# Optimization experiments

Hardware: AMD Instinct MI355X
Metric: run time of the kernel (lower is better)

Reference implementation:

```python
import jax, jax.numpy as jnp
import numpy as np

N_VERTS = 200000
N_TETS = 800000
FREQ_NUM = 4
SCALE = 1.0
HID = 256
D_IN = 3 + 6 * FREQ_NUM  # 27

_TRI_TABLE = np.array([
    [-1,-1,-1,-1,-1,-1],[1,0,2,-1,-1,-1],[4,0,3,-1,-1,-1],[1,4,2,1,3,4],
    [3,1,5,-1,-1,-1],[2,3,0,2,5,3],[1,4,0,1,5,4],[4,2,5,-1,-1,-1],
    [4,5,2,-1,-1,-1],[4,1,0,4,5,1],[3,2,0,3,5,2],[1,3,5,-1,-1,-1],
    [4,1,2,4,3,1],[3,0,4,-1,-1,-1],[2,0,1,-1,-1,-1],[-1,-1,-1,-1,-1,-1]], dtype=np.int32)
_NUM_TRI = np.array([0,1,1,2,1,2,2,1,1,2,2,1,2,1,1,0], dtype=np.int32)
_BASE_EDGES = np.array([0,1,0,2,0,3,1,2,1,3,2,3], dtype=np.int32)


def _pos_enc(x):
    feats = [x]
    for i in range(FREQ_NUM):
        f = float(2 ** i) * np.pi / SCALE
        feats.append(jnp.sin(f * x))
        feats.append(jnp.cos(f * x))
    return jnp.concatenate(feats, axis=-1)  # [N, 27]


def _mlp_sdf(pos, w0, b0, w1, b1, w2, b2, w3, b3, wf, bf):
    h = jax.nn.relu(_pos_enc(pos) @ w0 + b0)
    for w, b in ((w1, b1), (w2, b2), (w3, b3)):
        h = jax.nn.relu(h @ w + b)
    return (h @ wf + bf)[:, 0]  # [N]


def setup_inputs() -> dict:
    key = jax.random.key(0)
    ks = jax.random.split(key, 12)
    def lin(k, fan_in, shape):
        return jax.random.normal(k, shape, jnp.float32) * (2.0 / fan_in) ** 0.5
    return {
        "pos": jax.random.normal(ks[0], (N_VERTS, 3), jnp.float32),
        "tet_fx4": jax.random.randint(ks[1], (N_TETS, 4), 0, N_VERTS, dtype=jnp.int32),
        "w0": lin(ks[2], D_IN, (D_IN, HID)), "b0": jnp.zeros((HID,), jnp.float32),
        "w1": lin(ks[3], HID, (HID, HID)), "b1": jnp.zeros((HID,), jnp.float32),
        "w2": lin(ks[4], HID, (HID, HID)), "b2": jnp.zeros((HID,), jnp.float32),
        "w3": lin(ks[5], HID, (HID, HID)), "b3": jnp.zeros((HID,), jnp.float32),
        "wf": lin(ks[6], HID, (HID, 1)), "bf": jnp.zeros((1,), jnp.float32),
    }


def reference(pos, tet_fx4, w0, b0, w1, b1, w2, b2, w3, b3, wf, bf):
    # SDF from the positional-encoding MLP (DMTetGeometry)
    sdf = _mlp_sdf(pos, w0, b0, w1, b1, w2, b2, w3, b3, wf, bf)

    # --- marching tetrahedra (DMTet.__call__) ---
    occ = sdf > 0                       # [N]
    occ_fx4 = occ[tet_fx4]              # [F,4]
    occ_sum = occ_fx4.sum(-1)
    valid = (occ_sum > 0) & (occ_sum < 4)
    vt = tet_fx4[valid]                 # [V,4] tets crossed by the surface
    occ_v = occ_fx4[valid]              # [V,4]

    # all 6 edges per valid tet, sorted so (lo, hi)
    e = vt[:, _BASE_EDGES].reshape(-1, 2)                         # [6V,2]
    e = jnp.stack([jnp.minimum(e[:, 0], e[:, 1]),
                   jnp.maximum(e[:, 0], e[:, 1])], axis=1)
    uniq, inv = jnp.unique(e, axis=0, return_inverse=True)        # dedup edges
    inv = inv.reshape(-1)

    # edges whose endpoints straddle the zero level set
    cross = occ[uniq].sum(-1) == 1                                 # [U]
    mapping = jnp.where(cross, jnp.cumsum(cross) - 1, -1)          # compact ids
    idx_map = mapping[inv].reshape(-1, 6)                          # [V,6]
    interp_v = uniq[cross]                                         # [M,2]

    # linear interpolation of crossing vertices along each crossing edge
    p = pos[interp_v]                                              # [M,2,3]
    s = sdf[interp_v]                                              # [M,2]
    denom = s[:, 0] - s[:, 1]                                      # s0 + (-s1)
    verts = (p[:, 0] * (-s[:, 1])[:, None] + p[:, 1] * s[:, 0][:, None]) / denom[:, None]

    # triangle table lookup
    tetindex = (occ_v.astype(jnp.int32) * (2 ** jnp.arange(4, dtype=jnp.int32))).sum(-1)
    ntri = jnp.asarray(_NUM_TRI)[tetindex]
    tri = jnp.asarray(_TRI_TABLE)[tetindex]
    m1 = ntri == 1
    m2 = ntri == 2
    f1 = jnp.take_along_axis(idx_map[m1], tri[m1][:, :3], axis=1).reshape(-1, 3)
    f2 = jnp.take_along_axis(idx_map[m2], tri[m2][:, :6], axis=1).reshape(-1, 3)
    faces = jnp.concatenate([f1, f2], axis=0)
    return verts, faces
```

## Files before the change

### kernel.cpp

```cpp
#include <hip/hip_runtime.h>
#include <cstdint>
#include <cstddef>

#define NV 200000
#define NT 800000
#define ROWS 64
#define MBLK 3125
#define NBLK 3125
#define NSEGS 196
#define PCAP 4096
#define AST 264
#define PST (ROWS*AST)

typedef unsigned int u32;
typedef unsigned long long u64;

typedef __attribute__((ext_vector_type(8))) _Float16 half8;
typedef __attribute__((ext_vector_type(4))) float f32x4;
typedef __attribute__((ext_vector_type(16))) float f32x16;
#define MFMA32F __builtin_amdgcn_mfma_f32_32x32x16_f16

__constant__ int c_tri[16][6] = {
  {-1,-1,-1,-1,-1,-1},{1,0,2,-1,-1,-1},{4,0,3,-1,-1,-1},{1,4,2,1,3,4},
  {3,1,5,-1,-1,-1},{2,3,0,2,5,3},{1,4,0,1,5,4},{4,2,5,-1,-1,-1},
  {4,5,2,-1,-1,-1},{4,1,0,4,5,1},{3,2,0,3,5,2},{1,3,5,-1,-1,-1},
  {4,1,2,4,3,1},{3,0,4,-1,-1,-1},{2,0,1,-1,-1,-1},{-1,-1,-1,-1,-1,-1}};
__constant__ int c_ntri[16] = {0,1,1,2,1,2,2,1,1,2,2,1,2,1,1,0};
__constant__ int c_be[12] = {0,1,0,2,0,3,1,2,1,3,2,3};

__device__ __forceinline__ void split2(float x, _Float16& h, _Float16& m){
  h = (_Float16)x;
  const float r = x - (float)h;
  m = (_Float16)(r * 2048.0f);
}

__global__ void split_weights(const float* __restrict__ w0, const float* __restrict__ w1,
                              const float* __restrict__ w2, const float* __restrict__ w3,
                              _Float16* __restrict__ wp, u32* __restrict__ segcur)
{
  const int t = blockIdx.x*256 + threadIdx.x;
  if (t < 256) segcur[t] = 0u;
  int base, psz, c, kg, n, kvalid;
  const float* w;
  if (t < 1024){
    base = 0; psz = 8192;
    c = t >> 9; kg = (t >> 8) & 1; n = t & 255;
    w = w0; kvalid = 27;
  } else {
    int r = t - 1024;
    const int l = r >> 13;
    r &= 8191;
    c = r >> 9; kg = (r >> 8) & 1; n = r & 255;
    base = 16384 + l*131072; psz = 65536;
    w = (l==0) ? w1 : (l==1) ? w2 : w3;
    kvalid = 256;
  }
  half8 hv, mv;
#pragma unroll
  for (int j=0;j<8;j++){
    const int k = c*16 + kg*8 + j;
    const float val = (k < kvalid) ? w[k*256 + n] : 0.f;
    _Float16 h, m; split2(val, h, m);
    hv[j] = h; mv[j] = m;
  }
  const int off = (c*256 + n)*16 + kg*8;
  *(half8*)(wp + base + off) = hv;
  *(half8*)(wp + base + psz + off) = mv;
}

template<int NCH, int PSZ, bool LAST>
__device__ __forceinline__ void layer_run(
    const _Float16* __restrict__ Wl, const float* __restrict__ Bv,
    const float* __restrict__ wfv,
    _Float16 (*Af)[ROWS][AST], float (*part)[5],
    int lane, int wv)
{
  const int l31 = lane & 31, hi = lane >> 5;
  const int rt = wv >> 2, cg = wv & 3;
  const int col0 = cg * 64;
  f32x16 g0[2], g1[2];
#pragma unroll
  for (int nt=0; nt<2; nt++){
#pragma unroll
    for (int r=0; r<16; r++){ g0[nt][r] = 0.f; g1[nt][r] = 0.f; }
  }

  const _Float16* bp = Wl + (u32)((col0 + l31)*16 + hi*8);
  half8 bA[2][2], bB[2][2];

  auto loadB = [&](int c, half8 (*dst)[2]){
#pragma unroll
    for (int p=0;p<2;p++)
#pragma unroll
      for (int nt=0;nt<2;nt++)
        dst[p][nt] = *(const half8*)(bp + p*PSZ + c*4096 + nt*512);
  };
  auto compute = [&](int c, const half8 (*bb)[2]){
    const _Float16* ap = &Af[0][rt*32 + l31][c*16 + hi*8];
    const half8 ah = *(const half8*)(ap);
    const half8 am = *(const half8*)(ap + PST);
#pragma unroll
    for (int nt=0;nt<2;nt++){
      g0[nt] = MFMA32F(ah, bb[0][nt], g0[nt], 0,0,0);
      g1[nt] = MFMA32F(ah, bb[1][nt], g1[nt], 0,0,0);
      g1[nt] = MFMA32F(am, bb[0][nt], g1[nt], 0,0,0);
    }
  };

  loadB(0, bA);
#pragma unroll 1
  for (int ch=0; ch<NCH/2; ch++){
    const int c0 = 2*ch;
    loadB(c0+1, bB);
    compute(c0, bA);
    if (c0+2 < NCH) loadB(c0+2, bA);
    compute(c0+1, bB);
  }
  __syncthreads();

  const float S = 4.8828125e-4f;
  if (!LAST){
#pragma unroll
    for (int nt=0;nt<2;nt++){
      const int col = col0 + nt*32 + l31;
      const float bias = Bv[col];
#pragma unroll
      for (int reg=0;reg<16;reg++){
        const int row = rt*32 + (reg&3) + 8*(reg>>2) + 4*hi;
        const float v = fmaxf(g0[nt][reg] + S*g1[nt][reg] + bias, 0.f);
        _Float16 h,m; split2(v,h,m);
        Af[0][row][col] = h; Af[1][row][col] = m;
      }
    }
  } else {
    float pr[16];
#pragma unroll
    for (int reg=0;reg<16;reg++) pr[reg] = 0.f;
#pragma unroll
    for (int nt=0;nt<2;nt++){
      const int col = col0 + nt*32 + l31;
      const float bias = Bv[col];
      const float w = wfv[col];
#pragma unroll
      for (int reg=0;reg<16;reg++)
        pr[reg] += fmaxf(g0[nt][reg] + S*g1[nt][reg] + bias, 0.f) * w;
    }
#pragma unroll
    for (int s=1;s<32;s<<=1)
#pragma unroll
      for (int reg=0;reg<16;reg++)
        pr[reg] += __shfl_xor(pr[reg], s, 64);
    if (l31 == 0){
#pragma unroll
      for (int reg=0;reg<16;reg++)
        part[rt*32 + (reg&3) + 8*(reg>>2) + 4*hi][cg] = pr[reg];
    }
  }
  __syncthreads();
}

__global__ __launch_bounds__(512,4) void mlp_mfma(
    const float* __restrict__ pos, const _Float16* __restrict__ wp,
    const float* __restrict__ b0, const float* __restrict__ b1,
    const float* __restrict__ b2, const float* __restrict__ b3,
    const float* __restrict__ wf, const float* __restrict__ bf,
    float* __restrict__ sdf)
{
  __shared__ _Float16 Af[2][ROWS][AST];
  __shared__ float part[ROWS][5];
  const int tid = threadIdx.x;
  const int lane = tid & 63, wv = tid >> 6;
  const int row0 = blockIdx.x * ROWS;

#pragma unroll
  for (int it=0; it<4; it++){
    const int idx = it*512 + tid;
    const int r = idx & 63, f = idx >> 6;
    float val = 0.f;
    if (f < 3){
      val = pos[(row0 + r)*3 + f];
    } else if (f < 27){
      const int g = (f-3)/6, rem = (f-3)%6;
      const int d = rem % 3;
      const float x = pos[(row0 + r)*3 + d];
      const float fr = (float)(1 << g) * 3.14159265358979323846f;
      val = (rem < 3) ? sinf(fr*x) : cosf(fr*x);
    }
    _Float16 h,m; split2(val,h,m);
    Af[0][r][f] = h; Af[1][r][f] = m;
  }
  __syncthreads();

  layer_run< 2,  8192,false>(wp + 0,      b0, nullptr, Af, part, lane, wv);
  layer_run<16, 65536,false>(wp + 16384,  b1, nullptr, Af, part, lane, wv);
  layer_run<16, 65536,false>(wp + 147456, b2, nullptr, Af, part, lane, wv);
  layer_run<16, 65536,true >(wp + 278528, b3, wf,      Af, part, lane, wv);

  if (tid < ROWS){
    float s = part[tid][0] + part[tid][1] + part[tid][2] + part[tid][3];
    sdf[row0 + tid] = s + bf[0];
  }
}

__device__ __forceinline__ u32 wave_scan_incl(u32 v, int lane){
#pragma unroll
  for (int s=1;s<64;s<<=1){
    const u32 y = __shfl_up(v, s, 64);
    if (lane >= s) v += y;
  }
  return v;
}
__device__ __forceinline__ u32 block_scan_fast(u32 v, u32* sh4, int tid){
  const int lane = tid & 63, wv = tid >> 6;
  const u32 incl = wave_scan_incl(v, lane);
  if (lane == 63) sh4[wv] = incl;
  __syncthreads();
  u32 base = 0;
#pragma unroll
  for (int w=0;w<3;w++) if (w < wv) base += sh4[w];
  return incl + base;
}
__device__ __forceinline__ u64 bscan_u64(u64 v, u64* sh, int tid){
  sh[tid]=v; __syncthreads();
#pragma unroll
  for (int s=1;s<256;s<<=1){
    const u64 y = (tid>=s) ? sh[tid-s] : 0ull;
    __syncthreads();
    sh[tid] += y;
    __syncthreads();
  }
  return sh[tid];
}

__global__ void tet_pairs(const int* __restrict__ tet, const float* __restrict__ sdf,
    unsigned char* __restrict__ codes, u32* __restrict__ tscan, u32* __restrict__ tsum,
    u32* __restrict__ segcur, u64* __restrict__ pairs)
{
  __shared__ u32 sh4[4];
  const int tid = threadIdx.x;
  const int t = blockIdx.x*256 + tid;
  const int4 v = *(const int4*)(&tet[4*t]);
  const int o0 = sdf[v.x] > 0.f;
  const int o1 = sdf[v.y] > 0.f;
  const int o2 = sdf[v.z] > 0.f;
  const int o3 = sdf[v.w] > 0.f;
  const int code = o0 | (o1<<1) | (o2<<2) | (o3<<3);
  codes[t] = (unsigned char)code;
  const int nt = c_ntri[code];
  if (nt > 0){
    const int vv[4] = {v.x, v.y, v.z, v.w};
    const int oc[4] = {o0,o1,o2,o3};
#pragma unroll
    for (int e=0;e<6;e++){
      const int ia = c_be[2*e], ib = c_be[2*e+1];
      if (oc[ia] != oc[ib]){
        const int p = vv[ia], q = vv[ib];
        const int lo = p<q ? p : q, hi = p<q ? q : p;
        const int seg = lo >> 10;
        const u32 slot = atomicAdd(&segcur[seg], 1u);
        if (slot < PCAP)
          pairs[(size_t)seg*PCAP + slot] = ((u64)(u32)lo << 32) | (u32)hi;
      }
    }
  }
  const u32 my = (u32)(nt==1) | ((u32)(nt==2)<<16);
  const u32 incl = block_scan_fast(my, sh4, tid);
  tscan[t] = incl - my;
  if (tid == 255) tsum[blockIdx.x] = incl;
}

__global__ void seg_process(const u64* __restrict__ pairs_in, const u32* __restrict__ segcur,
    u64* __restrict__ uq, u32* __restrict__ ucnt, u32* __restrict__ ucnt_ex,
    u32* __restrict__ usum, const u32* __restrict__ tsum, u64* __restrict__ tsumE,
    u32* __restrict__ meta)
{
  const int tid = threadIdx.x;
  if (blockIdx.x == NSEGS){
    __shared__ u64 sh64[256];
    u64 loc[13]; u64 tot = 0ull;
#pragma unroll
    for (int i=0;i<13;i++){
      const int idx = tid*13 + i;
      const u32 p = (idx < NBLK) ? tsum[idx] : 0u;
      const u64 u = (u64)(p & 0xffffu) | ((u64)(p >> 16) << 32);
      loc[i] = u; tot += u;
    }
    const u64 incl = bscan_u64(tot, sh64, tid);
    u64 run = incl - tot;
#pragma unroll
    for (int i=0;i<13;i++){
      const int idx = tid*13 + i;
      if (idx < NBLK) tsumE[idx] = run;
      run += loc[i];
    }
    if (tid == 255){ meta[0] = (u32)(incl & 0xffffffffull); meta[1] = (u32)(incl >> 32); }
    return;
  }

  __shared__ u64 P[PCAP];
  __shared__ u32 sh4[4];
  __shared__ u32 shbase;
  const int seg = blockIdx.x;
  int n = (int)segcur[seg];
  if (n > PCAP) n = PCAP;
  int np = 1; while (np < n) np <<= 1;

  for (int i=tid; i<np; i+=256)
    P[i] = (i < n) ? pairs_in[(size_t)seg*PCAP + i] : ~0ull;
  if (tid == 0) shbase = 0u;
  __syncthreads();

  for (int k=2; k<=np; k<<=1){
    for (int j=k>>1; j>0; j>>=1){
      for (int i=tid; i<np; i+=256){
        const int ij = i ^ j;
        if (ij > i){
          const u64 a = P[i], b = P[ij];
          const bool up = ((i & k) == 0);
          if ((a > b) == up){ P[i] = b; P[ij] = a; }
        }
      }
      __syncthreads();
    }
  }

  for (int c=0; c<n; c+=256){
    const int i = c + tid;
    u64 key = 0ull; u32 f = 0u;
    if (i < n){
      key = P[i];
      f = (i == 0 || P[i] != P[i-1]) ? 1u : 0u;
    }
    __syncthreads();
    const u32 incl = block_scan_fast(f, sh4, tid);
    const u32 base = shbase;
    if (f) P[base + incl - 1u] = key;
    __syncthreads();
    if (tid == 255) shbase = base + incl;
    __syncthreads();
  }
  const int uc = (int)shbase;

  for (int i=tid; i<uc; i+=256) uq[(size_t)seg*PCAP + i] = P[i];

  const int lo0 = seg << 10;
  for (int c=0; c<1024; c+=256){
    const int lo = lo0 + c + tid;
    if (lo < NV){
      const u64 kl = (u64)(u32)lo << 32;
      const u64 kh = (u64)(u32)(lo+1) << 32;
      int a=0, b=uc;
      while (a < b){ const int m=(a+b)>>1; if (P[m] < kl) a=m+1; else b=m; }
      const int lb = a;
      b = uc;
      while (a < b){ const int m=(a+b)>>1; if (P[m] < kh) a=m+1; else b=m; }
      ucnt_ex[lo] = (u32)lb;
      ucnt[lo] = (u32)(a - lb);
    }
  }
  if (tid == 0) usum[seg] = (u32)uc;
}

__global__ void emit_all(const int* __restrict__ tet, const float* __restrict__ pos,
    const float* __restrict__ sdf, const unsigned char* __restrict__ codes,
    const u32* __restrict__ tscan, const u64* __restrict__ tsumE, const u32* __restrict__ meta,
    const u64* __restrict__ uq, const u32* __restrict__ ucnt, const u32* __restrict__ ucnt_ex,
    const u32* __restrict__ usum, float* __restrict__ out, int out_size)
{
  __shared__ u32 sh4[4];
  __shared__ u32 shu[NSEGS];
  __shared__ u32 shM;
  const int tid = threadIdx.x;
  {
    const u32 v = (tid < NSEGS) ? usum[tid] : 0u;
    const u32 incl = block_scan_fast(v, sh4, tid);
    if (tid < NSEGS) shu[tid] = incl - v;
    if (tid == NSEGS-1) shM = incl;
    __syncthreads();
  }

  if (blockIdx.x < NSEGS){
    const int seg = blockIdx.x;
    const int uc = (int)usum[seg];
    const u32 base = shu[seg];
    for (int i=tid; i<uc; i+=256){
      const u64 key = uq[(size_t)seg*PCAP + i];
      const int lo = (int)(key >> 32);
      const int hi = (int)(key & 0xffffffffull);
      const float s0 = sdf[lo], s1 = sdf[hi];
      const float d = s0 - s1;
      const float vx = (pos[3*lo  ]*(-s1) + pos[3*hi  ]*s0) / d;
      const float vy = (pos[3*lo+1]*(-s1) + pos[3*hi+1]*s0) / d;
      const float vz = (pos[3*lo+2]*(-s1) + pos[3*hi+2]*s0) / d;
      const long long w = 3ll*(long long)(base + (u32)i);
      if (w + 3 <= (long long)out_size){
        out[w] = vx; out[w+1] = vy; out[w+2] = vz;
      }
    }
  } else {
    const int t = (blockIdx.x - NSEGS)*256 + tid;
    const int code = codes[t];
    const int nt = c_ntri[code];
    if (nt == 0) return;
    const u64 tb = tsumE[t>>8];
    const u32 ts = tscan[t];
    const u32 n1e = (u32)(tb & 0xffffffffull) + (ts & 0xffffu);
    const u32 n2e = (u32)(tb >> 32) + (ts >> 16);
    const u32 N1 = meta[0];
    const u32 M  = shM;
    const u32 fb = (nt==1) ? n1e : (N1 + 2u*n2e);
    const int4 v = *(const int4*)(&tet[4*t]);
    const int vv[4] = {v.x, v.y, v.z, v.w};
    for (int r=0;r<nt;r++){
      for (int k=0;k<3;k++){
        const int e = c_tri[code][3*r+k];
        const int ia = c_be[2*e], ib = c_be[2*e+1];
        const int p = vv[ia], q = vv[ib];
        const int lo = p<q ? p : q, hi = p<q ? q : p;
        const int seg = lo >> 10;
        const u32 st = ucnt_ex[lo];
        const int u = (int)ucnt[lo];
        const u64* b = uq + (size_t)seg*PCAP + st;
        int id = -1;
        for (int j=0;j<u;j++){
          if ((int)(b[j] & 0xffffffffull) == hi){ id = (int)(shu[seg] + st) + j; break; }
        }
        const long long w = 3ll*(long long)M + 3ll*(long long)(fb + (u32)r) + k;
        if (w < (long long)out_size && id >= 0) out[w] = (float)id;
      }
    }
  }
}

extern "C" void kernel_launch(void* const* d_in, const int* in_sizes, int n_in,
                              void* d_out, int out_size, void* d_ws, size_t ws_size,
                              hipStream_t stream)
{
  (void)in_sizes; (void)n_in; (void)ws_size;
  const float* pos = (const float*)d_in[0];
  const int*   tet = (const int*)d_in[1];
  const float* w0 = (const float*)d_in[2];
  const float* b0 = (const float*)d_in[3];
  const float* w1 = (const float*)d_in[4];
  const float* b1 = (const float*)d_in[5];
  const float* w2 = (const float*)d_in[6];
  const float* b2 = (const float*)d_in[7];
  const float* w3 = (const float*)d_in[8];
  const float* b3 = (const float*)d_in[9];
  const float* wf = (const float*)d_in[10];
  const float* bf = (const float*)d_in[11];
  float* out = (float*)d_out;
  char* ws = (char*)d_ws;

  float*         sdf   = (float*)(ws + 0);
  unsigned char* codes = (unsigned char*)(ws + 800000);
  u32* tscan   = (u32*)(ws + 1600000);
  u32* tsum    = (u32*)(ws + 4800000);
  u64* tsumE   = (u64*)(ws + 4812800);
  u32* segcur  = (u32*)(ws + 4837888);
  u32* usum    = (u32*)(ws + 4838912);
  u32* meta    = (u32*)(ws + 4839936);
  u32* ucnt    = (u32*)(ws + 4840000);
  u32* ucnt_ex = (u32*)(ws + 5640000);
  _Float16* wp = (_Float16*)(ws + 6440000);
  u64* pairs   = (u64*)(ws + 7259200);

  split_weights<<<100,256,0,stream>>>(w0,w1,w2,w3,wp,segcur);
  mlp_mfma<<<MBLK,512,0,stream>>>(pos,wp,b0,b1,b2,b3,wf,bf,sdf);

  tet_pairs<<<NBLK,256,0,stream>>>(tet,sdf,codes,tscan,tsum,segcur,pairs);
  seg_process<<<NSEGS+1,256,0,stream>>>(pairs,segcur,pairs,ucnt,ucnt_ex,usum,tsum,tsumE,meta);
  emit_all<<<NSEGS+NBLK,256,0,stream>>>(tet,pos,sdf,codes,tscan,tsumE,meta,
                                        pairs,ucnt,ucnt_ex,usum,out,out_size);
}
```

Baseline: 497.5 us.

## Remap MLP waves to column strips and add 32-row tail blocks

Each of the 8 waves now owns a 32-column strip and loops over all row tiles, so every B weight fragment loaded from global memory is reused across two row tiles instead of each wave loading two column tiles. This halves per-wave weight loads while increasing A-fragment LDS reads. The grid is split into 3072 full 64-row blocks plus 106 half-size 32-row blocks, so the last wave of blocks is finer-grained and work spreads more evenly across CUs. Partial sums are now reduced across 8 waves instead of 4.

```diff
diff --git a/kernel.cpp b/kernel.cpp
--- a/kernel.cpp
+++ b/kernel.cpp
@@ -5,18 +5,17 @@
 #define NV 200000
 #define NT 800000
 #define ROWS 64
-#define MBLK 3125
+#define MAINB 3072
+#define TAILB 106
+#define MBLK (MAINB+TAILB)
 #define NBLK 3125
 #define NSEGS 196
 #define PCAP 4096
-#define AST 264
-#define PST (ROWS*AST)
 
 typedef unsigned int u32;
 typedef unsigned long long u64;
 
 typedef __attribute__((ext_vector_type(8))) _Float16 half8;
-typedef __attribute__((ext_vector_type(4))) float f32x4;
 typedef __attribute__((ext_vector_type(16))) float f32x16;
 #define MFMA32F __builtin_amdgcn_mfma_f32_32x32x16_f16
 
@@ -68,42 +67,38 @@
   *(half8*)(wp + base + psz + off) = mv;
 }
 
-template<int NCH, int PSZ, bool LAST>
+template<int RT, int NCH, int PSZ, bool LAST>
 __device__ __forceinline__ void layer_run(
     const _Float16* __restrict__ Wl, const float* __restrict__ Bv,
     const float* __restrict__ wfv,
-    _Float16 (*Af)[ROWS][AST], float (*part)[5],
+    _Float16* __restrict__ Af, float (*part)[8],
     int lane, int wv)
 {
   const int l31 = lane & 31, hi = lane >> 5;
-  const int rt = wv >> 2, cg = wv & 3;
-  const int col0 = cg * 64;
-  f32x16 g0[2], g1[2];
-#pragma unroll
-  for (int nt=0; nt<2; nt++){
-#pragma unroll
-    for (int r=0; r<16; r++){ g0[nt][r] = 0.f; g1[nt][r] = 0.f; }
-  }
+  const int col0 = wv * 32;
+  constexpr u32 PSTl = (u32)(RT*32*264);
+  f32x16 g0[RT], g1[RT];
+#pragma unroll
+  for (int i=0;i<RT;i++)
+#pragma unroll
+    for (int r=0;r<16;r++){ g0[i][r] = 0.f; g1[i][r] = 0.f; }
 
   const _Float16* bp = Wl + (u32)((col0 + l31)*16 + hi*8);
-  half8 bA[2][2], bB[2][2];
-
-  auto loadB = [&](int c, half8 (*dst)[2]){
-#pragma unroll
-    for (int p=0;p<2;p++)
-#pragma unroll
-      for (int nt=0;nt<2;nt++)
-        dst[p][nt] = *(const half8*)(bp + p*PSZ + c*4096 + nt*512);
+  half8 bA[2], bB[2];
+
+  auto loadB = [&](int c, half8* dst){
+    dst[0] = *(const half8*)(bp + c*4096);
+    dst[1] = *(const half8*)(bp + PSZ + c*4096);
   };
-  auto compute = [&](int c, const half8 (*bb)[2]){
-    const _Float16* ap = &Af[0][rt*32 + l31][c*16 + hi*8];
-    const half8 ah = *(const half8*)(ap);
-    const half8 am = *(const half8*)(ap + PST);
-#pragma unroll
-    for (int nt=0;nt<2;nt++){
-      g0[nt] = MFMA32F(ah, bb[0][nt], g0[nt], 0,0,0);
-      g1[nt] = MFMA32F(ah, bb[1][nt], g1[nt], 0,0,0);
-      g1[nt] = MFMA32F(am, bb[0][nt], g1[nt], 0,0,0);
+  auto compute = [&](int c, const half8* bb){
+#pragma unroll
+    for (int rt=0;rt<RT;rt++){
+      const _Float16* ap = Af + (u32)((rt*32 + l31)*264 + c*16 + hi*8);
+      const half8 ah = *(const half8*)(ap);
+      const half8 am = *(const half8*)(ap + PSTl);
+      g0[rt] = MFMA32F(ah, bb[0], g0[rt], 0,0,0);
+      g1[rt] = MFMA32F(ah, bb[1], g1[rt], 0,0,0);
+      g1[rt] = MFMA32F(am, bb[0], g1[rt], 0,0,0);
     }
   };
 
@@ -119,44 +114,56 @@
   __syncthreads();
 
   const float S = 4.8828125e-4f;
+  const int col = col0 + l31;
   if (!LAST){
-#pragma unroll
-    for (int nt=0;nt<2;nt++){
-      const int col = col0 + nt*32 + l31;
-      const float bias = Bv[col];
+    const float bias = Bv[col];
+#pragma unroll
+    for (int rt=0;rt<RT;rt++)
 #pragma unroll
       for (int reg=0;reg<16;reg++){
         const int row = rt*32 + (reg&3) + 8*(reg>>2) + 4*hi;
-        const float v = fmaxf(g0[nt][reg] + S*g1[nt][reg] + bias, 0.f);
+        const float v = fmaxf(g0[rt][reg] + S*g1[rt][reg] + bias, 0.f);
         _Float16 h,m; split2(v,h,m);
-        Af[0][row][col] = h; Af[1][row][col] = m;
+        Af[(u32)(row*264 + col)] = h;
+        Af[PSTl + (u32)(row*264 + col)] = m;
       }
-    }
   } else {
-    float pr[16];
-#pragma unroll
-    for (int reg=0;reg<16;reg++) pr[reg] = 0.f;
-#pragma unroll
-    for (int nt=0;nt<2;nt++){
-      const int col = col0 + nt*32 + l31;
-      const float bias = Bv[col];
-      const float w = wfv[col];
+    const float bias = Bv[col];
+    const float w = wfv[col];
+    float pr[RT][16];
+#pragma unroll
+    for (int rt=0;rt<RT;rt++)
 #pragma unroll
       for (int reg=0;reg<16;reg++)
-        pr[reg] += fmaxf(g0[nt][reg] + S*g1[nt][reg] + bias, 0.f) * w;
-    }
+        pr[rt][reg] = fmaxf(g0[rt][reg] + S*g1[rt][reg] + bias, 0.f) * w;
 #pragma unroll
     for (int s=1;s<32;s<<=1)
 #pragma unroll
-      for (int reg=0;reg<16;reg++)
-        pr[reg] += __shfl_xor(pr[reg], s, 64);
+      for (int rt=0;rt<RT;rt++)
+#pragma unroll
+        for (int reg=0;reg<16;reg++)
+          pr[rt][reg] += __shfl_xor(pr[rt][reg], s, 64);
     if (l31 == 0){
 #pragma unroll
-      for (int reg=0;reg<16;reg++)
-        part[rt*32 + (reg&3) + 8*(reg>>2) + 4*hi][cg] = pr[reg];
+      for (int rt=0;rt<RT;rt++)
+#pragma unroll
+        for (int reg=0;reg<16;reg++)
+          part[rt*32 + (reg&3) + 8*(reg>>2) + 4*hi][wv] = pr[rt][reg];
     }
   }
   __syncthreads();
+}
+
+__device__ __forceinline__ float posenc_val(const float* __restrict__ pos, int gr, int f){
+  if (f < 3) return pos[gr*3 + f];
+  if (f < 27){
+    const int g = (f-3)/6, rem = (f-3)%6;
+    const int d = rem % 3;
+    const float x = pos[gr*3 + d];
+    const float fr = (float)(1 << g) * 3.14159265358979323846f;
+    return (rem < 3) ? sinf(fr*x) : cosf(fr*x);
+  }
+  return 0.f;
 }
 
 __global__ __launch_bounds__(512,4) void mlp_mfma(
@@ -166,39 +173,60 @@
     const float* __restrict__ wf, const float* __restrict__ bf,
     float* __restrict__ sdf)
 {
-  __shared__ _Float16 Af[2][ROWS][AST];
-  __shared__ float part[ROWS][5];
+  __shared__ _Float16 Af[2*ROWS*264];
+  __shared__ float part[ROWS][8];
   const int tid = threadIdx.x;
   const int lane = tid & 63, wv = tid >> 6;
-  const int row0 = blockIdx.x * ROWS;
-
-#pragma unroll
-  for (int it=0; it<4; it++){
-    const int idx = it*512 + tid;
-    const int r = idx & 63, f = idx >> 6;
-    float val = 0.f;
-    if (f < 3){
-      val = pos[(row0 + r)*3 + f];
-    } else if (f < 27){
-      const int g = (f-3)/6, rem = (f-3)%6;
-      const int d = rem % 3;
-      const float x = pos[(row0 + r)*3 + d];
-      const float fr = (float)(1 << g) * 3.14159265358979323846f;
-      val = (rem < 3) ? sinf(fr*x) : cosf(fr*x);
-    }
-    _Float16 h,m; split2(val,h,m);
-    Af[0][r][f] = h; Af[1][r][f] = m;
-  }
-  __syncthreads();
-
-  layer_run< 2,  8192,false>(wp + 0,      b0, nullptr, Af, part, lane, wv);
-  layer_run<16, 65536,false>(wp + 16384,  b1, nullptr, Af, part, lane, wv);
-  layer_run<16, 65536,false>(wp + 147456, b2, nullptr, Af, part, lane, wv);
-  layer_run<16, 65536,true >(wp + 278528, b3, wf,      Af, part, lane, wv);
-
-  if (tid < ROWS){
-    float s = part[tid][0] + part[tid][1] + part[tid][2] + part[tid][3];
-    sdf[row0 + tid] = s + bf[0];
+  const int bid = blockIdx.x;
+
+  if (bid < MAINB){
+    const int row0 = bid * ROWS;
+#pragma unroll
+    for (int it=0; it<4; it++){
+      const int idx = it*512 + tid;
+      const int r = idx & 63, f = idx >> 6;
+      const float val = posenc_val(pos, row0 + r, f);
+      _Float16 h,m; split2(val,h,m);
+      Af[(u32)(r*264 + f)] = h;
+      Af[(u32)(ROWS*264 + r*264 + f)] = m;
+    }
+    __syncthreads();
+
+    layer_run<2, 2,  8192,false>(wp + 0,      b0, nullptr, Af, part, lane, wv);
+    layer_run<2,16, 65536,false>(wp + 16384,  b1, nullptr, Af, part, lane, wv);
+    layer_run<2,16, 65536,false>(wp + 147456, b2, nullptr, Af, part, lane, wv);
+    layer_run<2,16, 65536,true >(wp + 278528, b3, wf,      Af, part, lane, wv);
+
+    if (tid < ROWS){
+      float s = 0.f;
+#pragma unroll
+      for (int w=0; w<8; w++) s += part[tid][w];
+      sdf[row0 + tid] = s + bf[0];
+    }
+  } else {
+    const int row0 = MAINB*ROWS + (bid - MAINB) * 32;
+#pragma unroll
+    for (int it=0; it<2; it++){
+      const int idx = it*512 + tid;
+      const int r = idx & 31, f = idx >> 5;
+      const float val = posenc_val(pos, row0 + r, f);
+      _Float16 h,m; split2(val,h,m);
+      Af[(u32)(r*264 + f)] = h;
+      Af[(u32)(32*264 + r*264 + f)] = m;
+    }
+    __syncthreads();
+
+    layer_run<1, 2,  8192,false>(wp + 0,      b0, nullptr, Af, part, lane, wv);
+    layer_run<1,16, 65536,false>(wp + 16384,  b1, nullptr, Af, part, lane, wv);
+    layer_run<1,16, 65536,false>(wp + 147456, b2, nullptr, Af, part, lane, wv);
+    layer_run<1,16, 65536,true >(wp + 278528, b3, wf,      Af, part, lane, wv);
+
+    if (tid < 32){
+      float s = 0.f;
+#pragma unroll
+      for (int w=0; w<8; w++) s += part[tid][w];
+      sdf[row0 + tid] = s + bf[0];
+    }
   }
 }
 
```

Result: no change. 491.2 us (-1.3%).
